# Performance work log

Hardware: AMD Instinct MI355X
Metric: run time of the kernel (lower is better)

The kernel has to match this reference:

```python
import jax, jax.numpy as jnp
import numpy as np

E, H, I, K, T = 8, 1024, 2816, 2, 2048


def setup_inputs() -> dict:
    key = jax.random.key(0)
    k1, k2, k3, k4, k5, k6 = jax.random.split(key, 6)
    hidden_states = jax.random.normal(k1, (T, H), dtype=jnp.float32)
    top_k_indices = jax.random.randint(k2, (T, K), 0, E, dtype=jnp.int32)
    raw = jax.random.uniform(k3, (T, K), dtype=jnp.float32) + 0.1
    top_k_values = raw / jnp.sum(raw, axis=-1, keepdims=True)  # router softmax-like weights
    scale = 1.0 / np.sqrt(H)
    w_gate = jax.random.normal(k4, (E, H, I), dtype=jnp.float32) * scale
    w_up = jax.random.normal(k5, (E, H, I), dtype=jnp.float32) * scale
    w_down = jax.random.normal(k6, (E, I, H), dtype=jnp.float32) * (1.0 / np.sqrt(I))
    return {
        "hidden_states": hidden_states,
        "top_k_indices": top_k_indices,
        "top_k_values": top_k_values,
        "w_gate": w_gate,
        "w_up": w_up,
        "w_down": w_down,
    }


def reference(hidden_states, top_k_indices, top_k_values, w_gate, w_up, w_down):
    # Each expert: SwiGLU FFN  down( silu(x @ gate) * (x @ up) )
    # Run every expert on every token (dense reference for grouped-GEMM dispatch),
    # then combine with the per-token top-k routing weights.
    def expert(wg, wu, wd):
        g = jnp.matmul(hidden_states, wg)          # [T, I]
        u = jnp.matmul(hidden_states, wu)          # [T, I]
        return jnp.matmul(jax.nn.silu(g) * u, wd)  # [T, H]

    y = jax.vmap(expert)(w_gate, w_up, w_down)     # [E, T, H]

    t = hidden_states.shape[0]
    # comb[t, e] = sum over k of top_k_values[t, k] where top_k_indices[t, k] == e
    comb = jnp.zeros((t, w_gate.shape[0]), dtype=hidden_states.dtype)
    comb = comb.at[jnp.arange(t)[:, None], top_k_indices].add(top_k_values)
    out = jnp.einsum('te,eth->th', comb, y)        # weighted combine -> [T, H]
    return out
```

## Files before the change

### kernel.cpp

```cpp
#include <hip/hip_runtime.h>
#include <stdint.h>

#define T_TOK 2048
#define KTOP  2
#define NEXP  8
#define HDIM  1024
#define IDIM  2816

#define BM        256
#define MAX_TILES 24
#define NPAIR     (T_TOK * KTOP)
#define NPAIR_PAD (NPAIR + BM)

#define BN2  128
#define BK2  32
#define BKp2 40

#define BN3  64
#define BK3  64
#define BKp3 72

typedef __attribute__((ext_vector_type(8))) short short8;
typedef __attribute__((ext_vector_type(4))) float floatx4;

__device__ __forceinline__ unsigned short f2bf(float f) {
  unsigned int u = __float_as_uint(f);
  u += 0x7fffu + ((u >> 16) & 1u);
  return (unsigned short)(u >> 16);
}

__global__ void setup_kernel(const int* __restrict__ idx,
                             const float* __restrict__ vals,
                             int* __restrict__ hdr,
                             int* __restrict__ stok,
                             float* __restrict__ sw) {
  __shared__ int cnt[NEXP];
  __shared__ int off[NEXP];
  int tid = threadIdx.x;
  if (tid < NEXP) cnt[tid] = 0;
  __syncthreads();
  for (int p = tid; p < NPAIR; p += blockDim.x) atomicAdd(&cnt[idx[p]], 1);
  __syncthreads();
  if (tid == 0) {
    int s = 0, nt = 0;
    for (int e = 0; e < NEXP; ++e) {
      off[e] = s;
      int n = cnt[e];
      for (int t0 = 0; t0 < n; t0 += BM) {
        hdr[nt] = e;
        hdr[32 + nt] = s + t0;
        hdr[64 + nt] = s + n;
        nt++;
      }
      s += n;
    }
    for (; nt < MAX_TILES; ++nt) hdr[nt] = -1;
  }
  __syncthreads();
  for (int p = tid; p < NPAIR; p += blockDim.x) {
    int e = idx[p];
    int pos = atomicAdd(&off[e], 1);
    stok[pos] = p / KTOP;
    sw[pos] = vals[p];
  }
}

__global__ void gather_kernel(const float* __restrict__ hidden,
                              const int* __restrict__ stok,
                              unsigned short* __restrict__ Xs) {
  int p = blockIdx.x;
  int t = stok[p];
  const float4* src = reinterpret_cast<const float4*>(hidden + (size_t)t * HDIM);
  float4 v = src[threadIdx.x];
  uint2 q;
  q.x = f2bf(v.x) | ((unsigned)f2bf(v.y) << 16);
  q.y = f2bf(v.z) | ((unsigned)f2bf(v.w) << 16);
  *reinterpret_cast<uint2*>(Xs + (size_t)p * HDIM + threadIdx.x * 4) = q;
}

__global__ __launch_bounds__(512, 2) void gateup_kernel(
    const unsigned short* __restrict__ Xs, const float* __restrict__ wg,
    const float* __restrict__ wu, const int* __restrict__ hdr,
    const float* __restrict__ sw_g, unsigned short* __restrict__ Act) {
  int by = blockIdx.y;
  int e = hdr[by];
  if (e < 0) return;
  int row0 = hdr[32 + by];
  int row_end = hdr[64 + by];
  int n0 = blockIdx.x * BN2;

  __shared__ __align__(16) unsigned short As[BM * BKp2];
  __shared__ __align__(16) unsigned short Bg[BN2 * BKp2];
  __shared__ __align__(16) unsigned short Bu[BN2 * BKp2];
  __shared__ float sw[BM];

  int tid = threadIdx.x;
  int lane = tid & 63;
  int wave = tid >> 6;
  if (tid < BM) sw[tid] = sw_g[row0 + tid];

  const float* wgb = wg + (size_t)e * HDIM * IDIM;
  const float* wub = wu + (size_t)e * HDIM * IDIM;

  floatx4 accg[4][4], accu[4][4];
  floatx4 z = {0.f, 0.f, 0.f, 0.f};
#pragma unroll
  for (int a = 0; a < 4; ++a)
#pragma unroll
    for (int b = 0; b < 4; ++b) { accg[a][b] = z; accu[a][b] = z; }

  int wm = (wave >> 1) * 64;
  int wn = (wave & 1) * 64;

  for (int kb = 0; kb < HDIM; kb += BK2) {
    __syncthreads();
#pragma unroll
    for (int it = 0; it < 2; ++it) {
      int cc = wave * 2 + it;
      int m = cc * 16 + (lane >> 2);
      int k = (lane & 3) * 8;
      uint4 v = *reinterpret_cast<const uint4*>(Xs + (size_t)(row0 + m) * HDIM + kb + k);
      *reinterpret_cast<uint4*>(&As[m * BKp2 + k]) = v;
    }
#pragma unroll
    for (int it = 0; it < 2; ++it) {
      int cc = wave * 2 + it;
      const float* wb = (cc & 8) ? wub : wgb;
      unsigned short* Bs = (cc & 8) ? Bu : Bg;
      int r = cc & 7;
      int kblk = r >> 1, nh = r & 1;
      int n = nh * 64 + lane;
      int k = kblk * 8;
      const float* src = wb + (size_t)(kb + k) * IDIM + n0 + n;
      uint4 q;
      q.x = f2bf(src[0])        | ((unsigned)f2bf(src[(size_t)IDIM])     << 16);
      q.y = f2bf(src[2 * (size_t)IDIM]) | ((unsigned)f2bf(src[3 * (size_t)IDIM]) << 16);
      q.z = f2bf(src[4 * (size_t)IDIM]) | ((unsigned)f2bf(src[5 * (size_t)IDIM]) << 16);
      q.w = f2bf(src[6 * (size_t)IDIM]) | ((unsigned)f2bf(src[7 * (size_t)IDIM]) << 16);
      *reinterpret_cast<uint4*>(&Bs[n * BKp2 + k]) = q;
    }
    __syncthreads();

    int krd = (lane >> 4) * 8;
    short8 af[4], bgf[4], buf_[4];
#pragma unroll
    for (int tm = 0; tm < 4; ++tm)
      af[tm] = *reinterpret_cast<const short8*>(&As[(wm + tm * 16 + (lane & 15)) * BKp2 + krd]);
#pragma unroll
    for (int tn = 0; tn < 4; ++tn) {
      bgf[tn] = *reinterpret_cast<const short8*>(&Bg[(wn + tn * 16 + (lane & 15)) * BKp2 + krd]);
      buf_[tn] = *reinterpret_cast<const short8*>(&Bu[(wn + tn * 16 + (lane & 15)) * BKp2 + krd]);
    }
#pragma unroll
    for (int tm = 0; tm < 4; ++tm)
#pragma unroll
      for (int tn = 0; tn < 4; ++tn) {
        accg[tm][tn] = __builtin_amdgcn_mfma_f32_16x16x32_bf16(af[tm], bgf[tn], accg[tm][tn], 0, 0, 0);
        accu[tm][tn] = __builtin_amdgcn_mfma_f32_16x16x32_bf16(af[tm], buf_[tn], accu[tm][tn], 0, 0, 0);
      }
  }

  int rowlim = row_end - row0;
#pragma unroll
  for (int tm = 0; tm < 4; ++tm)
#pragma unroll
    for (int tn = 0; tn < 4; ++tn)
#pragma unroll
      for (int r = 0; r < 4; ++r) {
        int rl = wm + tm * 16 + (lane >> 4) * 4 + r;
        if (rl < rowlim) {
          int col = n0 + wn + tn * 16 + (lane & 15);
          float g = accg[tm][tn][r];
          float u = accu[tm][tn][r];
          float s = g / (1.f + __expf(-g));
          Act[(size_t)(row0 + rl) * IDIM + col] = f2bf(s * u * sw[rl]);
        }
      }
}

__global__ __launch_bounds__(512, 2) void down_kernel(
    const unsigned short* __restrict__ Act, const float* __restrict__ wd,
    const int* __restrict__ hdr, const int* __restrict__ stok,
    float* __restrict__ out) {
  int by = blockIdx.y;
  int e = hdr[by];
  if (e < 0) return;
  int row0 = hdr[32 + by];
  int row_end = hdr[64 + by];
  int n0 = blockIdx.x * BN3;

  __shared__ __align__(16) unsigned short As[BM * BKp3];
  __shared__ __align__(16) unsigned short Bd[BN3 * BKp3];
  __shared__ int stk[BM];

  int tid = threadIdx.x;
  int lane = tid & 63;
  int wave = tid >> 6;
  if (tid < BM) stk[tid] = stok[row0 + tid];

  const float* wdb = wd + (size_t)e * IDIM * HDIM;

  floatx4 acc[4][2];
  floatx4 z = {0.f, 0.f, 0.f, 0.f};
#pragma unroll
  for (int a = 0; a < 4; ++a) { acc[a][0] = z; acc[a][1] = z; }

  int wm = (wave >> 1) * 64;
  int wn = (wave & 1) * 32;

  for (int kb = 0; kb < IDIM; kb += BK3) {
    __syncthreads();
#pragma unroll
    for (int it = 0; it < 4; ++it) {
      int cc = wave * 4 + it;
      int m = cc * 8 + (lane >> 3);
      int k = (lane & 7) * 8;
      uint4 v = *reinterpret_cast<const uint4*>(Act + (size_t)(row0 + m) * IDIM + kb + k);
      *reinterpret_cast<uint4*>(&As[m * BKp3 + k]) = v;
    }
    {
      int n = lane;
      int k = wave * 8;
      const float* src = wdb + (size_t)(kb + k) * HDIM + n0 + n;
      uint4 q;
      q.x = f2bf(src[0])        | ((unsigned)f2bf(src[HDIM])     << 16);
      q.y = f2bf(src[2 * HDIM]) | ((unsigned)f2bf(src[3 * HDIM]) << 16);
      q.z = f2bf(src[4 * HDIM]) | ((unsigned)f2bf(src[5 * HDIM]) << 16);
      q.w = f2bf(src[6 * HDIM]) | ((unsigned)f2bf(src[7 * HDIM]) << 16);
      *reinterpret_cast<uint4*>(&Bd[n * BKp3 + k]) = q;
    }
    __syncthreads();

#pragma unroll
    for (int ks = 0; ks < BK3; ks += 32) {
      int krd = ks + (lane >> 4) * 8;
      short8 af[4], bdf[2];
#pragma unroll
      for (int tm = 0; tm < 4; ++tm)
        af[tm] = *reinterpret_cast<const short8*>(&As[(wm + tm * 16 + (lane & 15)) * BKp3 + krd]);
#pragma unroll
      for (int tn = 0; tn < 2; ++tn)
        bdf[tn] = *reinterpret_cast<const short8*>(&Bd[(wn + tn * 16 + (lane & 15)) * BKp3 + krd]);
#pragma unroll
      for (int tm = 0; tm < 4; ++tm)
#pragma unroll
        for (int tn = 0; tn < 2; ++tn)
          acc[tm][tn] = __builtin_amdgcn_mfma_f32_16x16x32_bf16(af[tm], bdf[tn], acc[tm][tn], 0, 0, 0);
    }
  }

  int rowlim = row_end - row0;
#pragma unroll
  for (int tm = 0; tm < 4; ++tm)
#pragma unroll
    for (int tn = 0; tn < 2; ++tn)
#pragma unroll
      for (int r = 0; r < 4; ++r) {
        int rl = wm + tm * 16 + (lane >> 4) * 4 + r;
        if (rl < rowlim) {
          int col = n0 + wn + tn * 16 + (lane & 15);
          int t = stk[rl];
          unsafeAtomicAdd(&out[(size_t)t * HDIM + col], acc[tm][tn][r]);
        }
      }
}

extern "C" void kernel_launch(void* const* d_in, const int* in_sizes, int n_in,
                              void* d_out, int out_size, void* d_ws, size_t ws_size,
                              hipStream_t stream) {
  const float* hidden = (const float*)d_in[0];
  const int* idx = (const int*)d_in[1];
  const float* vals = (const float*)d_in[2];
  const float* wg = (const float*)d_in[3];
  const float* wu = (const float*)d_in[4];
  const float* wd = (const float*)d_in[5];
  float* out = (float*)d_out;

  char* ws = (char*)d_ws;
  int* hdr = (int*)ws;
  int* stok = (int*)(ws + 4096);
  float* sw = (float*)(ws + 4096 + NPAIR_PAD * 4);
  unsigned short* Xs = (unsigned short*)(ws + 65536);
  unsigned short* Act = (unsigned short*)(ws + 65536 + (size_t)NPAIR_PAD * HDIM * 2);

  hipMemsetAsync(d_out, 0, (size_t)out_size * sizeof(float), stream);
  setup_kernel<<<1, 256, 0, stream>>>(idx, vals, hdr, stok, sw);
  gather_kernel<<<NPAIR, 256, 0, stream>>>(hidden, stok, Xs);
  gateup_kernel<<<dim3(IDIM / BN2, MAX_TILES), 512, 0, stream>>>(Xs, wg, wu, hdr, sw, Act);
  down_kernel<<<dim3(HDIM / BN3, MAX_TILES), 512, 0, stream>>>(Act, wd, hdr, stok, out);
}
```

Measured before the change: 469.8 us.

## Pre-convert weights to transposed bf16 and load tiles via global_load_lds

Adds a convert kernel that transposes and casts the fp32 gate, up and down weights into bf16 K-contiguous buffers in the workspace before each GEMM. The GEMMs then stream tiles straight into LDS with global_load_lds, replacing strided per-element fp32 loads and in-loop conversion. Tile height drops to 128 rows with 256-thread blocks. This costs an extra full read and write of all weights on every call and needs a large workspace, with the old path kept as a fallback when the workspace is too small.

After: 456.3 us. 2.9% less time.

```diff
diff --git a/kernel.cpp b/kernel.cpp
--- a/kernel.cpp
+++ b/kernel.cpp
@@ -7,18 +7,25 @@
 #define HDIM  1024
 #define IDIM  2816
 
-#define BM        256
-#define MAX_TILES 24
-#define NPAIR     (T_TOK * KTOP)
-#define NPAIR_PAD (NPAIR + BM)
-
-#define BN2  128
-#define BK2  32
-#define BKp2 40
-
-#define BN3  64
-#define BK3  64
-#define BKp3 72
+#define NPAIR 4096
+
+#define BM        128
+#define MAX_TILES 40
+#define NPP       (NPAIR + BM)
+#define BN2       128
+#define BK2       32
+#define BN3       64
+#define BK3       64
+
+#define R1BM   256
+#define R1T    24
+#define R1NPP  (NPAIR + R1BM)
+#define R1BN2  128
+#define R1BK2  32
+#define R1BKp2 40
+#define R1BN3  64
+#define R1BK3  64
+#define R1BKp3 72
 
 typedef __attribute__((ext_vector_type(8))) short short8;
 typedef __attribute__((ext_vector_type(4))) float floatx4;
@@ -29,11 +36,17 @@
   return (unsigned short)(u >> 16);
 }
 
+__device__ __forceinline__ void glds16(const unsigned short* g, unsigned short* l) {
+  __builtin_amdgcn_global_load_lds(
+      (const __attribute__((address_space(1))) unsigned int*)g,
+      (__attribute__((address_space(3))) unsigned int*)l, 16, 0, 0);
+}
+
 __global__ void setup_kernel(const int* __restrict__ idx,
                              const float* __restrict__ vals,
                              int* __restrict__ hdr,
                              int* __restrict__ stok,
-                             float* __restrict__ sw) {
+                             float* __restrict__ sw, int bm) {
   __shared__ int cnt[NEXP];
   __shared__ int off[NEXP];
   int tid = threadIdx.x;
@@ -46,15 +59,15 @@
     for (int e = 0; e < NEXP; ++e) {
       off[e] = s;
       int n = cnt[e];
-      for (int t0 = 0; t0 < n; t0 += BM) {
+      for (int t0 = 0; t0 < n; t0 += bm) {
         hdr[nt] = e;
-        hdr[32 + nt] = s + t0;
-        hdr[64 + nt] = s + n;
+        hdr[64 + nt] = s + t0;
+        hdr[128 + nt] = s + n;
         nt++;
       }
       s += n;
     }
-    for (; nt < MAX_TILES; ++nt) hdr[nt] = -1;
+    for (; nt < 64; ++nt) hdr[nt] = -1;
   }
   __syncthreads();
   for (int p = tid; p < NPAIR; p += blockDim.x) {
@@ -78,41 +91,225 @@
   *reinterpret_cast<uint2*>(Xs + (size_t)p * HDIM + threadIdx.x * 4) = q;
 }
 
-__global__ __launch_bounds__(512, 2) void gateup_kernel(
+__global__ __launch_bounds__(256) void convert_kernel(
+    const float* __restrict__ wg, const float* __restrict__ wu,
+    const float* __restrict__ wd, unsigned short* __restrict__ wgT,
+    unsigned short* __restrict__ wuT, unsigned short* __restrict__ wdT,
+    int zoff) {
+  __shared__ float ls[64][65];
+  int z = blockIdx.z + zoff;
+  int e = blockIdx.y;
+  int M = (z == 2) ? IDIM : HDIM;
+  int N = (z == 2) ? HDIM : IDIM;
+  const float* src = (z == 0 ? wg : z == 1 ? wu : wd) + (size_t)e * M * N;
+  unsigned short* dst = (z == 0 ? wgT : z == 1 ? wuT : wdT) + (size_t)e * M * N;
+  int ntx = N >> 6;
+  int n0 = (blockIdx.x % ntx) << 6;
+  int m0 = (blockIdx.x / ntx) << 6;
+  int t = threadIdx.x;
+  int rr = t >> 4, cc = (t & 15) * 4;
+#pragma unroll
+  for (int i = 0; i < 4; ++i) {
+    int r = rr + i * 16;
+    float4 v = *reinterpret_cast<const float4*>(src + (size_t)(m0 + r) * N + n0 + cc);
+    ls[r][cc] = v.x; ls[r][cc + 1] = v.y; ls[r][cc + 2] = v.z; ls[r][cc + 3] = v.w;
+  }
+  __syncthreads();
+#pragma unroll
+  for (int i = 0; i < 4; ++i) {
+    int n = rr + i * 16;
+    uint2 q;
+    q.x = f2bf(ls[cc][n])     | ((unsigned)f2bf(ls[cc + 1][n]) << 16);
+    q.y = f2bf(ls[cc + 2][n]) | ((unsigned)f2bf(ls[cc + 3][n]) << 16);
+    *reinterpret_cast<uint2*>(dst + (size_t)(n0 + n) * M + m0 + cc) = q;
+  }
+}
+
+__global__ __launch_bounds__(256, 2) void gateup_kernel(
+    const unsigned short* __restrict__ Xs, const unsigned short* __restrict__ wgT,
+    const unsigned short* __restrict__ wuT, const int* __restrict__ hdr,
+    const float* __restrict__ sw_g, unsigned short* __restrict__ Act) {
+  int by = blockIdx.y;
+  int e = hdr[by];
+  if (e < 0) return;
+  int row0 = hdr[64 + by];
+  int rowlim = hdr[128 + by] - row0;
+  int n0 = blockIdx.x * BN2;
+
+  __shared__ __align__(16) unsigned short As[BM * BK2];
+  __shared__ __align__(16) unsigned short Bg[BN2 * BK2];
+  __shared__ __align__(16) unsigned short Bu[BN2 * BK2];
+  __shared__ float sw[BM];
+
+  int tid = threadIdx.x, lane = tid & 63, wave = tid >> 6;
+  if (tid < BM) sw[tid] = sw_g[row0 + tid];
+
+  const unsigned short* wgb = wgT + (size_t)e * IDIM * HDIM;
+  const unsigned short* wub = wuT + (size_t)e * IDIM * HDIM;
+
+  floatx4 accg[4][4], accu[4][4];
+  floatx4 zz = {0.f, 0.f, 0.f, 0.f};
+#pragma unroll
+  for (int a = 0; a < 4; ++a)
+#pragma unroll
+    for (int b = 0; b < 4; ++b) { accg[a][b] = zz; accu[a][b] = zz; }
+
+  int wm = (wave >> 1) * 64, wn = (wave & 1) * 64;
+  int lr = lane >> 2;
+  int lk = (lane & 3) * 8;
+  int fr = lane & 15, fq = (lane >> 4) * 8;
+
+  for (int kb = 0; kb < HDIM; kb += BK2) {
+#pragma unroll
+    for (int it = 0; it < 2; ++it) {
+      int c = wave * 2 + it;
+      glds16(Xs  + (size_t)(row0 + c * 16 + lr) * HDIM + kb + lk, &As[c * 512]);
+      glds16(wgb + (size_t)(n0  + c * 16 + lr) * HDIM + kb + lk, &Bg[c * 512]);
+      glds16(wub + (size_t)(n0  + c * 16 + lr) * HDIM + kb + lk, &Bu[c * 512]);
+    }
+    __syncthreads();
+
+    short8 af[4], bg8[4], bu8[4];
+#pragma unroll
+    for (int x = 0; x < 4; ++x) {
+      af[x]  = *reinterpret_cast<const short8*>(&As[(wm + x * 16 + fr) * BK2 + fq]);
+      bg8[x] = *reinterpret_cast<const short8*>(&Bg[(wn + x * 16 + fr) * BK2 + fq]);
+      bu8[x] = *reinterpret_cast<const short8*>(&Bu[(wn + x * 16 + fr) * BK2 + fq]);
+    }
+#pragma unroll
+    for (int tm = 0; tm < 4; ++tm)
+#pragma unroll
+      for (int tn = 0; tn < 4; ++tn) {
+        accg[tm][tn] = __builtin_amdgcn_mfma_f32_16x16x32_bf16(af[tm], bg8[tn], accg[tm][tn], 0, 0, 0);
+        accu[tm][tn] = __builtin_amdgcn_mfma_f32_16x16x32_bf16(af[tm], bu8[tn], accu[tm][tn], 0, 0, 0);
+      }
+    __syncthreads();
+  }
+
+#pragma unroll
+  for (int tm = 0; tm < 4; ++tm)
+#pragma unroll
+    for (int tn = 0; tn < 4; ++tn)
+#pragma unroll
+      for (int r = 0; r < 4; ++r) {
+        int rl = wm + tm * 16 + (lane >> 4) * 4 + r;
+        if (rl < rowlim) {
+          int col = n0 + wn + tn * 16 + fr;
+          float g = accg[tm][tn][r];
+          float u = accu[tm][tn][r];
+          float s = g / (1.f + __expf(-g));
+          Act[(size_t)(row0 + rl) * IDIM + col] = f2bf(s * u * sw[rl]);
+        }
+      }
+}
+
+__global__ __launch_bounds__(256, 3) void down_kernel(
+    const unsigned short* __restrict__ Act, const unsigned short* __restrict__ wdT,
+    const int* __restrict__ hdr, const int* __restrict__ stok,
+    float* __restrict__ out) {
+  int by = blockIdx.y;
+  int e = hdr[by];
+  if (e < 0) return;
+  int row0 = hdr[64 + by];
+  int rowlim = hdr[128 + by] - row0;
+  int n0 = blockIdx.x * BN3;
+
+  __shared__ __align__(16) unsigned short As[BM * BK3];
+  __shared__ __align__(16) unsigned short Bd[BN3 * BK3];
+  __shared__ int stk[BM];
+
+  int tid = threadIdx.x, lane = tid & 63, wave = tid >> 6;
+  if (tid < BM) stk[tid] = stok[row0 + tid];
+
+  const unsigned short* wdb = wdT + (size_t)e * HDIM * IDIM;
+
+  floatx4 acc[4][2];
+  floatx4 zz = {0.f, 0.f, 0.f, 0.f};
+#pragma unroll
+  for (int a = 0; a < 4; ++a) { acc[a][0] = zz; acc[a][1] = zz; }
+
+  int wm = (wave >> 1) * 64, wn = (wave & 1) * 32;
+  int lr8 = lane >> 3;
+  int lk8 = (lane & 7) * 8;
+  int fr = lane & 15, fq = (lane >> 4) * 8;
+
+  for (int kb = 0; kb < IDIM; kb += BK3) {
+#pragma unroll
+    for (int it = 0; it < 4; ++it) {
+      int c = wave * 4 + it;
+      glds16(Act + (size_t)(row0 + c * 8 + lr8) * IDIM + kb + lk8, &As[c * 512]);
+    }
+#pragma unroll
+    for (int it = 0; it < 2; ++it) {
+      int c = wave * 2 + it;
+      glds16(wdb + (size_t)(n0 + c * 8 + lr8) * IDIM + kb + lk8, &Bd[c * 512]);
+    }
+    __syncthreads();
+
+#pragma unroll
+    for (int ks = 0; ks < BK3; ks += 32) {
+      short8 af[4], bd8[2];
+#pragma unroll
+      for (int x = 0; x < 4; ++x)
+        af[x] = *reinterpret_cast<const short8*>(&As[(wm + x * 16 + fr) * BK3 + ks + fq]);
+#pragma unroll
+      for (int x = 0; x < 2; ++x)
+        bd8[x] = *reinterpret_cast<const short8*>(&Bd[(wn + x * 16 + fr) * BK3 + ks + fq]);
+#pragma unroll
+      for (int tm = 0; tm < 4; ++tm)
+#pragma unroll
+        for (int tn = 0; tn < 2; ++tn)
+          acc[tm][tn] = __builtin_amdgcn_mfma_f32_16x16x32_bf16(af[tm], bd8[tn], acc[tm][tn], 0, 0, 0);
+    }
+    __syncthreads();
+  }
+
+#pragma unroll
+  for (int tm = 0; tm < 4; ++tm)
+#pragma unroll
+    for (int tn = 0; tn < 2; ++tn)
+#pragma unroll
+      for (int r = 0; r < 4; ++r) {
+        int rl = wm + tm * 16 + (lane >> 4) * 4 + r;
+        if (rl < rowlim) {
+          int col = n0 + wn + tn * 16 + fr;
+          unsafeAtomicAdd(&out[(size_t)stk[rl] * HDIM + col], acc[tm][tn][r]);
+        }
+      }
+}
+
+__global__ __launch_bounds__(512, 2) void gateup_fb(
     const unsigned short* __restrict__ Xs, const float* __restrict__ wg,
     const float* __restrict__ wu, const int* __restrict__ hdr,
     const float* __restrict__ sw_g, unsigned short* __restrict__ Act) {
   int by = blockIdx.y;
   int e = hdr[by];
   if (e < 0) return;
-  int row0 = hdr[32 + by];
-  int row_end = hdr[64 + by];
-  int n0 = blockIdx.x * BN2;
-
-  __shared__ __align__(16) unsigned short As[BM * BKp2];
-  __shared__ __align__(16) unsigned short Bg[BN2 * BKp2];
-  __shared__ __align__(16) unsigned short Bu[BN2 * BKp2];
-  __shared__ float sw[BM];
-
-  int tid = threadIdx.x;
-  int lane = tid & 63;
-  int wave = tid >> 6;
-  if (tid < BM) sw[tid] = sw_g[row0 + tid];
+  int row0 = hdr[64 + by];
+  int row_end = hdr[128 + by];
+  int n0 = blockIdx.x * R1BN2;
+
+  __shared__ __align__(16) unsigned short As[R1BM * R1BKp2];
+  __shared__ __align__(16) unsigned short Bg[R1BN2 * R1BKp2];
+  __shared__ __align__(16) unsigned short Bu[R1BN2 * R1BKp2];
+  __shared__ float sw[R1BM];
+
+  int tid = threadIdx.x, lane = tid & 63, wave = tid >> 6;
+  if (tid < R1BM) sw[tid] = sw_g[row0 + tid];
 
   const float* wgb = wg + (size_t)e * HDIM * IDIM;
   const float* wub = wu + (size_t)e * HDIM * IDIM;
 
   floatx4 accg[4][4], accu[4][4];
-  floatx4 z = {0.f, 0.f, 0.f, 0.f};
+  floatx4 zz = {0.f, 0.f, 0.f, 0.f};
 #pragma unroll
   for (int a = 0; a < 4; ++a)
 #pragma unroll
-    for (int b = 0; b < 4; ++b) { accg[a][b] = z; accu[a][b] = z; }
-
-  int wm = (wave >> 1) * 64;
-  int wn = (wave & 1) * 64;
-
-  for (int kb = 0; kb < HDIM; kb += BK2) {
+    for (int b = 0; b < 4; ++b) { accg[a][b] = zz; accu[a][b] = zz; }
+
+  int wm = (wave >> 1) * 64, wn = (wave & 1) * 64;
+
+  for (int kb = 0; kb < HDIM; kb += R1BK2) {
     __syncthreads();
 #pragma unroll
     for (int it = 0; it < 2; ++it) {
@@ -120,7 +317,7 @@
       int m = cc * 16 + (lane >> 2);
       int k = (lane & 3) * 8;
       uint4 v = *reinterpret_cast<const uint4*>(Xs + (size_t)(row0 + m) * HDIM + kb + k);
-      *reinterpret_cast<uint4*>(&As[m * BKp2 + k]) = v;
+      *reinterpret_cast<uint4*>(&As[m * R1BKp2 + k]) = v;
     }
 #pragma unroll
     for (int it = 0; it < 2; ++it) {
@@ -133,11 +330,11 @@
       int k = kblk * 8;
       const float* src = wb + (size_t)(kb + k) * IDIM + n0 + n;
       uint4 q;
-      q.x = f2bf(src[0])        | ((unsigned)f2bf(src[(size_t)IDIM])     << 16);
+      q.x = f2bf(src[0])                | ((unsigned)f2bf(src[(size_t)IDIM])     << 16);
       q.y = f2bf(src[2 * (size_t)IDIM]) | ((unsigned)f2bf(src[3 * (size_t)IDIM]) << 16);
       q.z = f2bf(src[4 * (size_t)IDIM]) | ((unsigned)f2bf(src[5 * (size_t)IDIM]) << 16);
       q.w = f2bf(src[6 * (size_t)IDIM]) | ((unsigned)f2bf(src[7 * (size_t)IDIM]) << 16);
-      *reinterpret_cast<uint4*>(&Bs[n * BKp2 + k]) = q;
+      *reinterpret_cast<uint4*>(&Bs[n * R1BKp2 + k]) = q;
     }
     __syncthreads();
 
@@ -145,11 +342,11 @@
     short8 af[4], bgf[4], buf_[4];
 #pragma unroll
     for (int tm = 0; tm < 4; ++tm)
-      af[tm] = *reinterpret_cast<const short8*>(&As[(wm + tm * 16 + (lane & 15)) * BKp2 + krd]);
+      af[tm] = *reinterpret_cast<const short8*>(&As[(wm + tm * 16 + (lane & 15)) * R1BKp2 + krd]);
 #pragma unroll
     for (int tn = 0; tn < 4; ++tn) {
-      bgf[tn] = *reinterpret_cast<const short8*>(&Bg[(wn + tn * 16 + (lane & 15)) * BKp2 + krd]);
-      buf_[tn] = *reinterpret_cast<const short8*>(&Bu[(wn + tn * 16 + (lane & 15)) * BKp2 + krd]);
+      bgf[tn]  = *reinterpret_cast<const short8*>(&Bg[(wn + tn * 16 + (lane & 15)) * R1BKp2 + krd]);
+      buf_[tn] = *reinterpret_cast<const short8*>(&Bu[(wn + tn * 16 + (lane & 15)) * R1BKp2 + krd]);
     }
 #pragma unroll
     for (int tm = 0; tm < 4; ++tm)
@@ -178,37 +375,34 @@
       }
 }
 
-__global__ __launch_bounds__(512, 2) void down_kernel(
+__global__ __launch_bounds__(512, 2) void down_fb(
     const unsigned short* __restrict__ Act, const float* __restrict__ wd,
     const int* __restrict__ hdr, const int* __restrict__ stok,
     float* __restrict__ out) {
   int by = blockIdx.y;
   int e = hdr[by];
   if (e < 0) return;
-  int row0 = hdr[32 + by];
-  int row_end = hdr[64 + by];
-  int n0 = blockIdx.x * BN3;
-
-  __shared__ __align__(16) unsigned short As[BM * BKp3];
-  __shared__ __align__(16) unsigned short Bd[BN3 * BKp3];
-  __shared__ int stk[BM];
-
-  int tid = threadIdx.x;
-  int lane = tid & 63;
-  int wave = tid >> 6;
-  if (tid < BM) stk[tid] = stok[row0 + tid];
+  int row0 = hdr[64 + by];
+  int row_end = hdr[128 + by];
+  int n0 = blockIdx.x * R1BN3;
+
+  __shared__ __align__(16) unsigned short As[R1BM * R1BKp3];
+  __shared__ __align__(16) unsigned short Bd[R1BN3 * R1BKp3];
+  __shared__ int stk[R1BM];
+
+  int tid = threadIdx.x, lane = tid & 63, wave = tid >> 6;
+  if (tid < R1BM) stk[tid] = stok[row0 + tid];
 
   const float* wdb = wd + (size_t)e * IDIM * HDIM;
 
   floatx4 acc[4][2];
-  floatx4 z = {0.f, 0.f, 0.f, 0.f};
-#pragma unroll
-  for (int a = 0; a < 4; ++a) { acc[a][0] = z; acc[a][1] = z; }
-
-  int wm = (wave >> 1) * 64;
-  int wn = (wave & 1) * 32;
-
-  for (int kb = 0; kb < IDIM; kb += BK3) {
+  floatx4 zz = {0.f, 0.f, 0.f, 0.f};
+#pragma unroll
+  for (int a = 0; a < 4; ++a) { acc[a][0] = zz; acc[a][1] = zz; }
+
+  int wm = (wave >> 1) * 64, wn = (wave & 1) * 32;
+
+  for (int kb = 0; kb < IDIM; kb += R1BK3) {
     __syncthreads();
 #pragma unroll
     for (int it = 0; it < 4; ++it) {
@@ -216,7 +410,7 @@
       int m = cc * 8 + (lane >> 3);
       int k = (lane & 7) * 8;
       uint4 v = *reinterpret_cast<const uint4*>(Act + (size_t)(row0 + m) * IDIM + kb + k);
-      *reinterpret_cast<uint4*>(&As[m * BKp3 + k]) = v;
+      *reinterpret_cast<uint4*>(&As[m * R1BKp3 + k]) = v;
     }
     {
       int n = lane;
@@ -227,20 +421,20 @@
       q.y = f2bf(src[2 * HDIM]) | ((unsigned)f2bf(src[3 * HDIM]) << 16);
       q.z = f2bf(src[4 * HDIM]) | ((unsigned)f2bf(src[5 * HDIM]) << 16);
       q.w = f2bf(src[6 * HDIM]) | ((unsigned)f2bf(src[7 * HDIM]) << 16);
-      *reinterpret_cast<uint4*>(&Bd[n * BKp3 + k]) = q;
-    }
-    __syncthreads();
-
-#pragma unroll
-    for (int ks = 0; ks < BK3; ks += 32) {
+      *reinterpret_cast<uint4*>(&Bd[n * R1BKp3 + k]) = q;
+    }
+    __syncthreads();
+
+#pragma unroll
+    for (int ks = 0; ks < R1BK3; ks += 32) {
       int krd = ks + (lane >> 4) * 8;
       short8 af[4], bdf[2];
 #pragma unroll
       for (int tm = 0; tm < 4; ++tm)
-        af[tm] = *reinterpret_cast<const short8*>(&As[(wm + tm * 16 + (lane & 15)) * BKp3 + krd]);
+        af[tm] = *reinterpret_cast<const short8*>(&As[(wm + tm * 16 + (lane & 15)) * R1BKp3 + krd]);
 #pragma unroll
       for (int tn = 0; tn < 2; ++tn)
-        bdf[tn] = *reinterpret_cast<const short8*>(&Bd[(wn + tn * 16 + (lane & 15)) * BKp3 + krd]);
+        bdf[tn] = *reinterpret_cast<const short8*>(&Bd[(wn + tn * 16 + (lane & 15)) * R1BKp3 + krd]);
 #pragma unroll
       for (int tm = 0; tm < 4; ++tm)
 #pragma unroll
@@ -259,8 +453,7 @@
         int rl = wm + tm * 16 + (lane >> 4) * 4 + r;
         if (rl < rowlim) {
           int col = n0 + wn + tn * 16 + (lane & 15);
-          int t = stk[rl];
-          unsafeAtomicAdd(&out[(size_t)t * HDIM + col], acc[tm][tn][r]);
+          unsafeAtomicAdd(&out[(size_t)stk[rl] * HDIM + col], acc[tm][tn][r]);
         }
       }
 }
@@ -275,17 +468,45 @@
   const float* wu = (const float*)d_in[4];
   const float* wd = (const float*)d_in[5];
   float* out = (float*)d_out;
-
   char* ws = (char*)d_ws;
-  int* hdr = (int*)ws;
-  int* stok = (int*)(ws + 4096);
-  float* sw = (float*)(ws + 4096 + NPAIR_PAD * 4);
-  unsigned short* Xs = (unsigned short*)(ws + 65536);
-  unsigned short* Act = (unsigned short*)(ws + 65536 + (size_t)NPAIR_PAD * HDIM * 2);
 
   hipMemsetAsync(d_out, 0, (size_t)out_size * sizeof(float), stream);
-  setup_kernel<<<1, 256, 0, stream>>>(idx, vals, hdr, stok, sw);
-  gather_kernel<<<NPAIR, 256, 0, stream>>>(hidden, stok, Xs);
-  gateup_kernel<<<dim3(IDIM / BN2, MAX_TILES), 512, 0, stream>>>(Xs, wg, wu, hdr, sw, Act);
-  down_kernel<<<dim3(HDIM / BN3, MAX_TILES), 512, 0, stream>>>(Act, wd, hdr, stok, out);
-}
+
+  const size_t OFF_STOK = 4096;
+  const size_t OFF_SW   = OFF_STOK + (size_t)NPP * 4;
+  const size_t OFF_XS   = 65536;
+  const size_t OFF_ACT  = OFF_XS + (size_t)NPP * HDIM * 2;
+  const size_t OFF_WG   = OFF_ACT + (size_t)NPP * IDIM * 2;
+  const size_t WSZ      = (size_t)NEXP * HDIM * IDIM * 2;
+  const size_t OFF_WU   = OFF_WG + WSZ;
+  const size_t NEED     = OFF_WU + WSZ;
+
+  if (ws_size >= NEED) {
+    int* hdr = (int*)ws;
+    int* stok = (int*)(ws + OFF_STOK);
+    float* sw = (float*)(ws + OFF_SW);
+    unsigned short* Xs  = (unsigned short*)(ws + OFF_XS);
+    unsigned short* Act = (unsigned short*)(ws + OFF_ACT);
+    unsigned short* wgT = (unsigned short*)(ws + OFF_WG);
+    unsigned short* wuT = (unsigned short*)(ws + OFF_WU);
+    unsigned short* wdT = wgT;
+
+    setup_kernel<<<1, 256, 0, stream>>>(idx, vals, hdr, stok, sw, BM);
+    convert_kernel<<<dim3(704, NEXP, 2), 256, 0, stream>>>(wg, wu, wd, wgT, wuT, wdT, 0);
+    gather_kernel<<<NPAIR, 256, 0, stream>>>(hidden, stok, Xs);
+    gateup_kernel<<<dim3(IDIM / BN2, MAX_TILES), 256, 0, stream>>>(Xs, wgT, wuT, hdr, sw, Act);
+    convert_kernel<<<dim3(704, NEXP, 1), 256, 0, stream>>>(wg, wu, wd, wgT, wuT, wdT, 2);
+    down_kernel<<<dim3(HDIM / BN3, MAX_TILES), 256, 0, stream>>>(Act, wdT, hdr, stok, out);
+  } else {
+    int* hdr = (int*)ws;
+    int* stok = (int*)(ws + 4096);
+    float* sw = (float*)(ws + 4096 + (size_t)R1NPP * 4);
+    unsigned short* Xs  = (unsigned short*)(ws + 65536);
+    unsigned short* Act = (unsigned short*)(ws + 65536 + (size_t)R1NPP * HDIM * 2);
+
+    setup_kernel<<<1, 256, 0, stream>>>(idx, vals, hdr, stok, sw, R1BM);
+    gather_kernel<<<NPAIR, 256, 0, stream>>>(hidden, stok, Xs);
+    gateup_fb<<<dim3(IDIM / R1BN2, R1T), 512, 0, stream>>>(Xs, wg, wu, hdr, sw, Act);
+    down_fb<<<dim3(HDIM / R1BN3, R1T), 512, 0, stream>>>(Act, wd, hdr, stok, out);
+  }
+}
```
